# Optimization experiments

Measured on AMD Instinct MI355X. Metric: run time of the kernel, lower is better.

Reference implementation:

```python
import jax, jax.numpy as jnp
import numpy as np

PLANES, RATIO = 512, 4
Q = PLANES // RATIO  # 128
B, H, W = 4, 128, 128


def _dw_stride2(x, k):
    # depthwise 3x3 stride-2 conv, NCHW, kernel [C,1,3,3]
    return jax.lax.conv_general_dilated(
        x, k, window_strides=(2, 2), padding=((1, 1), (1, 1)),
        feature_group_count=x.shape[1],
        dimension_numbers=('NCHW', 'OIHW', 'NCHW'))


def _upsample_bilinear_ac(x, out_h, out_w):
    # bilinear, align_corners=True (matches F.interpolate)
    n, c, h, w = x.shape
    def co(out, ins):
        s = (ins - 1) / (out - 1)
        pos = jnp.arange(out, dtype=jnp.float32) * jnp.float32(s)
        i0 = jnp.floor(pos).astype(jnp.int32)
        i1 = jnp.minimum(i0 + 1, ins - 1)
        return i0, i1, pos - i0.astype(jnp.float32)
    y0, y1, ty = co(out_h, h)
    x0, x1, tx = co(out_w, w)
    rows = x[:, :, y0, :] * (1 - ty)[None, None, :, None] + x[:, :, y1, :] * ty[None, None, :, None]
    return rows[:, :, :, x0] * (1 - tx) + rows[:, :, :, x1] * tx


def setup_inputs() -> dict:
    key = jax.random.key(0)
    ks = jax.random.split(key, 32)
    nrm = lambda k, s, sc=0.05: jax.random.normal(k, s, jnp.float32) * sc
    uni = lambda k, s: jax.random.uniform(k, s, jnp.float32, 0.5, 1.5)
    return {
        'feat': jax.random.normal(ks[0], (B, PLANES, H, W), jnp.float32),
        'w_phi': nrm(ks[1], (2 * Q, PLANES)),
        'bn_phi_s': uni(ks[2], (2 * Q,)), 'bn_phi_b': nrm(ks[3], (2 * Q,)),
        'w_theta': nrm(ks[4], (Q, PLANES)),
        'bn_theta_s': uni(ks[5], (Q,)), 'bn_theta_b': nrm(ks[6], (Q,)),
        'w_adj': nrm(ks[7], (Q, Q)),
        'bn_adj_s': uni(ks[8], (Q,)), 'bn_adj_b': nrm(ks[9], (Q,)),
        'w_wg': nrm(ks[10], (2 * Q, 2 * Q)),
        'bn_wg_s': uni(ks[11], (2 * Q,)), 'bn_wg_b': nrm(ks[12], (2 * Q,)),
        'w_conv3': nrm(ks[13], (PLANES, 2 * Q)),
        'bn3_s': uni(ks[14], (PLANES,)), 'bn3_b': nrm(ks[15], (PLANES,)),
        'w_local1': nrm(ks[16], (PLANES, 1, 3, 3), 0.2),
        'bnl1_s': uni(ks[17], (PLANES,)), 'bnl1_b': nrm(ks[18], (PLANES,)),
        'w_local2': nrm(ks[19], (PLANES, 1, 3, 3), 0.2),
        'bnl2_s': uni(ks[20], (PLANES,)), 'bnl2_b': nrm(ks[21], (PLANES,)),
        'w_local3': nrm(ks[22], (PLANES, 1, 3, 3), 0.2),
        'bnl3_s': uni(ks[23], (PLANES,)), 'bnl3_b': nrm(ks[24], (PLANES,)),
        'gamma': nrm(ks[25], (1,), 0.5),
        'w_final': nrm(ks[26], (PLANES, 2 * PLANES)),
        'bnf_s': uni(ks[27], (PLANES,)), 'bnf_b': nrm(ks[28], (PLANES,)),
    }


def reference(feat, w_phi, bn_phi_s, bn_phi_b, w_theta, bn_theta_s, bn_theta_b,
              w_adj, bn_adj_s, bn_adj_b, w_wg, bn_wg_s, bn_wg_b,
              w_conv3, bn3_s, bn3_b,
              w_local1, bnl1_s, bnl1_b, w_local2, bnl2_s, bnl2_b,
              w_local3, bnl3_s, bnl3_b, gamma, w_final, bnf_s, bnf_b):
    n, c, h, w = feat.shape
    bn2 = lambda x, s, b: x * s[None, :, None, None] + b[None, :, None, None]
    bn1 = lambda x, s, b: x * s[None, :, None] + b[None, :, None]
    conv1x1 = lambda x, wt: jnp.einsum('oc,nchw->nohw', wt, x)

    l = bn2(_dw_stride2(feat, w_local1), bnl1_s, bnl1_b)
    l = bn2(_dw_stride2(l, w_local2), bnl2_s, bnl2_b)
    l = bn2(_dw_stride2(l, w_local3), bnl3_s, bnl3_b)
    nl, cl, hl, wl = l.shape
    v = l.reshape(nl, cl, hl * wl)                      # [n,C,hw]
    energy = jnp.einsum('nck,ndk->ncd', v, v)           # [n,C,C]
    attn = jax.nn.softmax(jnp.max(energy, -1, keepdims=True) - energy, axis=-1)
    cam = jnp.einsum('ncd,ndk->nck', attn, v).reshape(nl, cl, hl, wl)
    l = gamma * cam + l
    local = _upsample_bilinear_ac(l, h, w)
    spatial_local_feat = feat * local + feat

    # ---- graph branch
    q = w_theta.shape[0]
    x_sqz = bn2(conv1x1(feat, w_phi), bn_phi_s, bn_phi_b).reshape(n, 2 * q, h * w)
    b_m = bn2(conv1x1(feat, w_theta), bn_theta_s, bn_theta_b).reshape(n, q, h * w)
    z_idt = jnp.einsum('nck,ndk->ncd', x_sqz, b_m)      # [n,2q,q]
    z = jnp.swapaxes(z_idt, 1, 2)                       # [n,q,2q]
    z = bn1(jnp.einsum('oi,nil->nol', w_adj, z), bn_adj_s, bn_adj_b)
    z = jnp.swapaxes(z, 1, 2) + z_idt                   # [n,2q,q]
    z = bn1(jnp.einsum('oi,nil->nol', w_wg, z), bn_wg_s, bn_wg_b)
    y = jnp.einsum('ncd,ndk->nck', z, b_m).reshape(n, 2 * q, h, w)
    y = bn2(conv1x1(y, w_conv3), bn3_s, bn3_b)
    g_out = jax.nn.relu(feat + y)

    out = bn2(conv1x1(jnp.concatenate([spatial_local_feat, g_out], axis=1), w_final), bnf_s, bnf_b)
    return out
```

## Files before the change

### kernel.cpp

```cpp
#include <hip/hip_runtime.h>
#include <hip/hip_bf16.h>
#include <cstddef>
#include <cstdint>

static constexpr int NB  = 4;
static constexpr int CH  = 512;
static constexpr int HH  = 128;
static constexpr int WWi = 128;
static constexpr int HW  = HH * WWi;
static constexpr int Qd  = 128;
static constexpr int Q2d = 256;

typedef __attribute__((ext_vector_type(8))) short bf8;
typedef __attribute__((ext_vector_type(4))) float f4;

__device__ __forceinline__ short f2bf(float x) {
  __hip_bfloat16 h = __float2bfloat16(x);
  short s; __builtin_memcpy(&s, &h, 2); return s;
}
__device__ __forceinline__ float bfs2f(short u) {
  union { unsigned int i; float f; } x;
  x.i = ((unsigned int)(unsigned short)u) << 16; return x.f;
}

__launch_bounds__(256)
__global__ void dw_conv_bn4(const float* __restrict__ in, float* __restrict__ out,
                            const float* __restrict__ wgt, const float* __restrict__ s,
                            const float* __restrict__ b, int Hi, int Wi, int Ho, int Wo4) {
  int idx = blockIdx.x * 256 + threadIdx.x;
  int q = idx % Wo4; int t = idx / Wo4;
  int ho = t % Ho; t /= Ho;
  int c = t % CH;
  const float* ip = in + (size_t)t * Hi * Wi;
  const float* wp = wgt + c * 9;
  float w[9];
#pragma unroll
  for (int k = 0; k < 9; k++) w[k] = wp[k];
  const int x0 = q * 8;
  float acc0 = 0.f, acc1 = 0.f, acc2 = 0.f, acc3 = 0.f;
#pragma unroll
  for (int kh = 0; kh < 3; kh++) {
    int y = ho * 2 - 1 + kh;
    if ((unsigned)y < (unsigned)Hi) {
      const float* row = ip + (size_t)y * Wi + x0;
      float4 v0 = *(const float4*)row;
      float4 v1 = *(const float4*)(row + 4);
      float left = (x0 > 0) ? row[-1] : 0.f;
      float xs[9] = {left, v0.x, v0.y, v0.z, v0.w, v1.x, v1.y, v1.z, v1.w};
      const float w0 = w[kh * 3 + 0], w1 = w[kh * 3 + 1], w2 = w[kh * 3 + 2];
      acc0 += w0 * xs[0] + w1 * xs[1] + w2 * xs[2];
      acc1 += w0 * xs[2] + w1 * xs[3] + w2 * xs[4];
      acc2 += w0 * xs[4] + w1 * xs[5] + w2 * xs[6];
      acc3 += w0 * xs[6] + w1 * xs[7] + w2 * xs[8];
    }
  }
  const float sc = s[c], bb = b[c];
  float4 o;
  o.x = acc0 * sc + bb; o.y = acc1 * sc + bb;
  o.z = acc2 * sc + bb; o.w = acc3 * sc + bb;
  *(float4*)(out + (size_t)idx * 4) = o;
}

__launch_bounds__(256)
__global__ void lrow_kernel(const float* __restrict__ lcam, float* __restrict__ lrow) {
  int idx = blockIdx.x * 256 + threadIdx.x;
  int wcol = idx & 127; int t = idx >> 7;
  int hy = t & 15; t >>= 4;
  float pos = wcol * (15.f / 127.f);
  int x0 = (int)pos; if (x0 > 15) x0 = 15;
  float tx = pos - x0;
  int x1 = x0 + 1; if (x1 > 15) x1 = 15;
  const float* lc = lcam + ((size_t)t * 16 + hy) * 16;
  lrow[idx] = lc[x0] * (1.f - tx) + lc[x1] * tx;
}

__launch_bounds__(256)
__global__ void cvt_f32_bf16(const float* __restrict__ in, short* __restrict__ out, int n4) {
  int i = blockIdx.x * 256 + threadIdx.x;
  if (i >= n4) return;
  float4 v = ((const float4*)in)[i];
  short tmp[4] = {f2bf(v.x), f2bf(v.y), f2bf(v.z), f2bf(v.w)};
  short4 o; __builtin_memcpy(&o, tmp, 8);
  ((short4*)out)[i] = o;
}

__launch_bounds__(256)
__global__ void slf_build(const float* __restrict__ feat, const float* __restrict__ lrw,
                          short* __restrict__ slfb, int h0) {
  int idx = blockIdx.x * 256 + threadIdx.x;
  int w8 = (idx & 15) * 8; int t = idx >> 4;
  int h = (t & 63) + h0; t >>= 6;
  const float posy = h * (15.f / 127.f);
  int hy0 = (int)posy; if (hy0 > 15) hy0 = 15;
  int hy1 = hy0 + 1; if (hy1 > 15) hy1 = 15;
  const float tyv = posy - hy0;
  const float* fr = feat + (size_t)t * HW + h * WWi + w8;
  const float* l0r = lrw + ((size_t)t * 16 + hy0) * WWi + w8;
  const float* l1r = lrw + ((size_t)t * 16 + hy1) * WWi + w8;
  float4 f0 = *(const float4*)fr, f1 = *(const float4*)(fr + 4);
  float4 a0 = *(const float4*)l0r, a1 = *(const float4*)(l0r + 4);
  float4 b0 = *(const float4*)l1r, b1 = *(const float4*)(l1r + 4);
  float fv[8], av[8], bv[8];
  __builtin_memcpy(&fv[0], &f0, 16); __builtin_memcpy(&fv[4], &f1, 16);
  __builtin_memcpy(&av[0], &a0, 16); __builtin_memcpy(&av[4], &a1, 16);
  __builtin_memcpy(&bv[0], &b0, 16); __builtin_memcpy(&bv[4], &b1, 16);
  union { short s[8]; bf8 v; } u;
#pragma unroll
  for (int e = 0; e < 8; e++) {
    float v = fv[e] * (1.f + av[e] + (bv[e] - av[e]) * tyv);
    u.s[e] = f2bf(v);
  }
  *(bf8*)(slfb + ((size_t)t * 64 + (h - h0)) * WWi + w8) = u.v;
}

__device__ __forceinline__ int sls(int row, int slot) {
  return row * 64 + ((slot ^ (((row >> 1) ^ (row >> 3)) & 7)) << 3);
}
__device__ __forceinline__ void stg64_b16(const short* __restrict__ src, size_t stride,
                                          int kb, short* lds, int t) {
#pragma unroll
  for (int i = 0; i < 4; i++) {
    int chunk = t + i * 256;
    int row = chunk >> 3, slot = chunk & 7;
    bf8 v = *(const bf8*)(src + (size_t)row * stride + kb + slot * 8);
    *(bf8*)(lds + sls(row, slot)) = v;
  }
}
__device__ __forceinline__ void stg64_f32(const float* __restrict__ src, size_t stride,
                                          int kb, short* lds, int t) {
#pragma unroll
  for (int i = 0; i < 4; i++) {
    int chunk = t + i * 256;
    int row = chunk >> 3, slot = chunk & 7;
    const float* sp = src + (size_t)row * stride + kb + slot * 8;
    float4 v0 = *(const float4*)sp, v1 = *(const float4*)(sp + 4);
    union { short s[8]; bf8 v; } u;
    u.s[0] = f2bf(v0.x); u.s[1] = f2bf(v0.y); u.s[2] = f2bf(v0.z); u.s[3] = f2bf(v0.w);
    u.s[4] = f2bf(v1.x); u.s[5] = f2bf(v1.y); u.s[6] = f2bf(v1.z); u.s[7] = f2bf(v1.w);
    *(bf8*)(lds + sls(row, slot)) = u.v;
  }
}
__device__ __forceinline__ void stg64_t32(const float* __restrict__ src, size_t sstride,
                                          int pb, short* lds, int t) {
#pragma unroll
  for (int i2 = 0; i2 < 4; i2++) {
    int chunk = t + i2 * 256;
    int c = (chunk >> 3) & 63;
    int p8 = ((chunk & 7) | ((chunk >> 6) & 8)) * 8;
    const float* fr = src + (size_t)c * sstride + pb + p8;
    float4 f0 = *(const float4*)fr, f1 = *(const float4*)(fr + 4);
    float fv[8];
    __builtin_memcpy(&fv[0], &f0, 16); __builtin_memcpy(&fv[4], &f1, 16);
    int slot = c >> 3, eidx = c & 7;
#pragma unroll
    for (int e = 0; e < 8; e++) {
      lds[sls(p8 + e, slot) + eidx] = f2bf(fv[e]);
    }
  }
}
__device__ __forceinline__ void stg64_t16(const short* __restrict__ src, size_t sstride,
                                          int pb, short* lds, int t) {
#pragma unroll
  for (int i2 = 0; i2 < 4; i2++) {
    int chunk = t + i2 * 256;
    int c = (chunk >> 3) & 63;
    int p8 = ((chunk & 7) | ((chunk >> 6) & 8)) * 8;
    bf8 v = *(const bf8*)(src + (size_t)c * sstride + pb + p8);
    int slot = c >> 3, eidx = c & 7;
#pragma unroll
    for (int e = 0; e < 8; e++) {
      lds[sls(p8 + e, slot) + eidx] = v[e];
    }
  }
}
__device__ __forceinline__ bf8 fragld64(const short* lds, int row, int kk, int lg) {
  return *(const bf8*)(lds + sls(row, kk * 4 + lg));
}

__launch_bounds__(256)
__global__ void energy_mfma(const float* __restrict__ l3, float* __restrict__ energy) {
  const int c0 = blockIdx.x * 128;
  const int d0 = blockIdx.y * 128;
  const int n = blockIdx.z;
  const int t = threadIdx.x;
  const int lane16 = t & 15, lg = (t >> 4) & 3, wave = t >> 6;
  const int wm = (wave >> 1) * 64, wn = (wave & 1) * 64;
  __shared__ __align__(16) short lA[8192], lB[8192];
  const float* srcA = l3 + ((size_t)n * CH + c0) * 256;
  const float* srcB = l3 + ((size_t)n * CH + d0) * 256;
  f4 acc[4][4];
#pragma unroll
  for (int i = 0; i < 4; i++)
#pragma unroll
    for (int j = 0; j < 4; j++) acc[i][j] = (f4)0.f;
  for (int kb = 0; kb < 256; kb += 64) {
    stg64_f32(srcA, 256, kb, lA, t);
    stg64_f32(srcB, 256, kb, lB, t);
    __syncthreads();
#pragma unroll
    for (int kk = 0; kk < 2; kk++) {
      bf8 av[4], bv[4];
#pragma unroll
      for (int i = 0; i < 4; i++) av[i] = fragld64(lA, wm + i * 16 + lane16, kk, lg);
#pragma unroll
      for (int j = 0; j < 4; j++) bv[j] = fragld64(lB, wn + j * 16 + lane16, kk, lg);
#pragma unroll
      for (int i = 0; i < 4; i++)
#pragma unroll
        for (int j = 0; j < 4; j++)
          acc[i][j] = __builtin_amdgcn_mfma_f32_16x16x32_bf16(av[i], bv[j], acc[i][j], 0, 0, 0);
    }
    __syncthreads();
  }
#pragma unroll
  for (int i = 0; i < 4; i++)
#pragma unroll
    for (int j = 0; j < 4; j++) {
      int d = d0 + wn + j * 16 + lane16;
#pragma unroll
      for (int r = 0; r < 4; r++) {
        int c = c0 + wm + i * 16 + lg * 4 + r;
        energy[((size_t)n * CH + c) * CH + d] = acc[i][j][r];
      }
    }
}

__launch_bounds__(256)
__global__ void softmax_attn(float* __restrict__ energy) {
  float* row = energy + (size_t)blockIdx.x * CH;
  int t = threadIdx.x;
  __shared__ float red[256];
  float e0 = row[t], e1 = row[t + 256];
  red[t] = fminf(e0, e1);
  __syncthreads();
  for (int s = 128; s > 0; s >>= 1) {
    if (t < s) red[t] = fminf(red[t], red[t + s]);
    __syncthreads();
  }
  float emin = red[0];
  __syncthreads();
  float w0 = __expf(emin - e0), w1 = __expf(emin - e1);
  red[t] = w0 + w1;
  __syncthreads();
  for (int s = 128; s > 0; s >>= 1) {
    if (t < s) red[t] += red[t + s];
    __syncthreads();
  }
  float inv = 1.f / red[0];
  row[t] = w0 * inv;
  row[t + 256] = w1 * inv;
}

__launch_bounds__(256)
__global__ void cam_mfma(const float* __restrict__ attn, const float* __restrict__ l3,
                         const float* __restrict__ gamma, float* __restrict__ lcam) {
  const int pb = blockIdx.x * 128;
  const int mb = blockIdx.y * 128;
  const int n = blockIdx.z;
  const int t = threadIdx.x;
  const int lane16 = t & 15, lg = (t >> 4) & 3, wave = t >> 6;
  const int wm = (wave >> 1) * 64, wn = (wave & 1) * 64;
  __shared__ __align__(16) short lA[8192], lB[8192];
  const float* srcA = attn + ((size_t)n * CH + mb) * CH;
  const float gm = gamma[0];
  f4 acc[4][4];
#pragma unroll
  for (int i = 0; i < 4; i++)
#pragma unroll
    for (int j = 0; j < 4; j++) acc[i][j] = (f4)0.f;
  for (int kb = 0; kb < 512; kb += 64) {
    stg64_f32(srcA, CH, kb, lA, t);
    stg64_t32(l3 + ((size_t)n * CH + kb) * 256, 256, pb, lB, t);
    __syncthreads();
#pragma unroll
    for (int kk = 0; kk < 2; kk++) {
      bf8 av[4], bv[4];
#pragma unroll
      for (int i = 0; i < 4; i++) av[i] = fragld64(lA, wm + i * 16 + lane16, kk, lg);
#pragma unroll
      for (int j = 0; j < 4; j++) bv[j] = fragld64(lB, wn + j * 16 + lane16, kk, lg);
#pragma unroll
      for (int i = 0; i < 4; i++)
#pragma unroll
        for (int j = 0; j < 4; j++)
          acc[i][j] = __builtin_amdgcn_mfma_f32_16x16x32_bf16(av[i], bv[j], acc[i][j], 0, 0, 0);
    }
    __syncthreads();
  }
#pragma unroll
  for (int i = 0; i < 4; i++)
#pragma unroll
    for (int j = 0; j < 4; j++) {
      int p = pb + wn + j * 16 + lane16;
#pragma unroll
      for (int r = 0; r < 4; r++) {
        int c = mb + wm + i * 16 + lg * 4 + r;
        size_t idx = ((size_t)n * CH + c) * 256 + p;
        lcam[idx] = gm * acc[i][j][r] + l3[idx];
      }
    }
}

__launch_bounds__(256)
__global__ void theta_mfma2(const short* __restrict__ wthb, const float* __restrict__ feat,
                            const float* __restrict__ s, const float* __restrict__ b,
                            short* __restrict__ bmb) {
  const int pb = blockIdx.x * 128;
  const int n = blockIdx.y;
  const int t = threadIdx.x;
  const int lane16 = t & 15, lg = (t >> 4) & 3, wave = t >> 6;
  const int wm = (wave >> 1) * 64, wn = (wave & 1) * 64;
  __shared__ __align__(16) short lA[8192], lB[8192];
  f4 acc[4][4];
#pragma unroll
  for (int i = 0; i < 4; i++)
#pragma unroll
    for (int j = 0; j < 4; j++) acc[i][j] = (f4)0.f;
  for (int kb = 0; kb < 512; kb += 64) {
    stg64_b16(wthb, 512, kb, lA, t);
    stg64_t32(feat + ((size_t)(n * CH) + kb) * HW, HW, pb, lB, t);
    __syncthreads();
#pragma unroll
    for (int kk = 0; kk < 2; kk++) {
      bf8 av[4], bv[4];
#pragma unroll
      for (int i = 0; i < 4; i++) av[i] = fragld64(lA, wm + i * 16 + lane16, kk, lg);
#pragma unroll
      for (int j = 0; j < 4; j++) bv[j] = fragld64(lB, wn + j * 16 + lane16, kk, lg);
#pragma unroll
      for (int i = 0; i < 4; i++)
#pragma unroll
        for (int j = 0; j < 4; j++)
          acc[i][j] = __builtin_amdgcn_mfma_f32_16x16x32_bf16(av[i], bv[j], acc[i][j], 0, 0, 0);
    }
    __syncthreads();
  }
#pragma unroll
  for (int i = 0; i < 4; i++)
#pragma unroll
    for (int j = 0; j < 4; j++) {
      int p = pb + wn + j * 16 + lane16;
#pragma unroll
      for (int r = 0; r < 4; r++) {
        int d = wm + i * 16 + lg * 4 + r;
        bmb[((size_t)(n * Qd) + d) * HW + p] = f2bf(s[d] * acc[i][j][r] + b[d]);
      }
    }
}

__launch_bounds__(256)
__global__ void rowsum_bf(const short* __restrict__ bmb, float* __restrict__ rs) {
  int row = blockIdx.x;
  int t = threadIdx.x;
  const short* r = bmb + (size_t)row * HW;
  float a = 0.f;
  for (int p = t * 8; p < HW; p += 2048) {
    bf8 v = *(const bf8*)(r + p);
#pragma unroll
    for (int e = 0; e < 8; e++) a += bfs2f(v[e]);
  }
  __shared__ float red[256];
  red[t] = a;
  __syncthreads();
  for (int s = 128; s > 0; s >>= 1) {
    if (t < s) red[t] += red[t + s];
    __syncthreads();
  }
  if (t == 0) rs[row] = red[0];
}

__launch_bounds__(256)
__global__ void m1_mfma2(const float* __restrict__ feat, const short* __restrict__ bmb,
                         float* __restrict__ m1p) {
  const int c0 = blockIdx.x * 128;
  const int kc = blockIdx.y;
  const int n = blockIdx.z;
  const int t = threadIdx.x;
  const int lane16 = t & 15, lg = (t >> 4) & 3, wave = t >> 6;
  const int wm = (wave >> 1) * 64, wn = (wave & 1) * 64;
  __shared__ __align__(16) short lA[8192], lB[8192];
  const float* srcA = feat + ((size_t)(n * CH) + c0) * HW;
  const short* srcB = bmb + (size_t)(n * Qd) * HW;
  f4 acc[4][4];
#pragma unroll
  for (int i = 0; i < 4; i++)
#pragma unroll
    for (int j = 0; j < 4; j++) acc[i][j] = (f4)0.f;
  const int kend = kc * 512 + 512;
  for (int kb = kc * 512; kb < kend; kb += 64) {
    stg64_f32(srcA, HW, kb, lA, t);
    stg64_b16(srcB, HW, kb, lB, t);
    __syncthreads();
#pragma unroll
    for (int kk = 0; kk < 2; kk++) {
      bf8 av[4], bv[4];
#pragma unroll
      for (int i = 0; i < 4; i++) av[i] = fragld64(lA, wm + i * 16 + lane16, kk, lg);
#pragma unroll
      for (int j = 0; j < 4; j++) bv[j] = fragld64(lB, wn + j * 16 + lane16, kk, lg);
#pragma unroll
      for (int i = 0; i < 4; i++)
#pragma unroll
        for (int j = 0; j < 4; j++)
          acc[i][j] = __builtin_amdgcn_mfma_f32_16x16x32_bf16(av[i], bv[j], acc[i][j], 0, 0, 0);
    }
    __syncthreads();
  }
#pragma unroll
  for (int i = 0; i < 4; i++)
#pragma unroll
    for (int j = 0; j < 4; j++) {
      int d = wn + j * 16 + lane16;
#pragma unroll
      for (int r = 0; r < 4; r++) {
        int c = c0 + wm + i * 16 + lg * 4 + r;
        m1p[(((size_t)kc * NB + n) * CH + c) * Qd + d] = acc[i][j][r];
      }
    }
}

__launch_bounds__(256)
__global__ void m1_reduce(const float* __restrict__ m1p, float* __restrict__ m1) {
  int idx = blockIdx.x * 256 + threadIdx.x;
  float a = 0.f;
#pragma unroll
  for (int kc = 0; kc < 32; kc++) a += m1p[(size_t)kc * (NB * CH * Qd) + idx];
  m1[idx] = a;
}

__launch_bounds__(128)
__global__ void zidt_kernel(const float* __restrict__ m1, const float* __restrict__ wphi,
                            const float* __restrict__ sp, const float* __restrict__ bp,
                            const float* __restrict__ rs, float* __restrict__ zidt) {
  int n = blockIdx.y, c = blockIdx.x, d = threadIdx.x;
  __shared__ float wrow[512];
  for (int i = d; i < 512; i += 128) wrow[i] = wphi[(size_t)c * 512 + i];
  __syncthreads();
  const float* mb = m1 + (size_t)n * CH * Qd;
  float acc = 0.f;
#pragma unroll 4
  for (int i = 0; i < 512; i++) acc += wrow[i] * mb[i * Qd + d];
  zidt[((size_t)n * Q2d + c) * Qd + d] = sp[c] * acc + bp[c] * rs[n * Qd + d];
}

__launch_bounds__(128)
__global__ void z3_kernel(const float* __restrict__ zidt, const float* __restrict__ wadj,
                          const float* __restrict__ sa, const float* __restrict__ ba,
                          float* __restrict__ z3) {
  int n = blockIdx.y, c = blockIdx.x, d = threadIdx.x;
  __shared__ float zr[128];
  zr[d] = zidt[((size_t)n * Q2d + c) * Qd + d];
  __syncthreads();
  const float* wrow = wadj + (size_t)d * 128;
  float acc = 0.f;
#pragma unroll 4
  for (int i = 0; i < 128; i++) acc += wrow[i] * zr[i];
  z3[((size_t)n * Q2d + c) * Qd + d] = sa[d] * acc + ba[d] + zr[d];
}

__launch_bounds__(128)
__global__ void z4_kernel(const float* __restrict__ z3, const float* __restrict__ wwg,
                          const float* __restrict__ sw, const float* __restrict__ bw,
                          float* __restrict__ z4) {
  int n = blockIdx.y, o = blockIdx.x, d = threadIdx.x;
  __shared__ float wrow[256];
  wrow[d] = wwg[(size_t)o * 256 + d];
  wrow[d + 128] = wwg[(size_t)o * 256 + 128 + d];
  __syncthreads();
  const float* zb = z3 + (size_t)n * Q2d * Qd;
  float acc = 0.f;
#pragma unroll 4
  for (int i = 0; i < 256; i++) acc += wrow[i] * zb[i * Qd + d];
  z4[((size_t)n * Q2d + o) * Qd + d] = sw[o] * acc + bw[o];
}

__launch_bounds__(128)
__global__ void wz_kernel(const float* __restrict__ z4, const float* __restrict__ wc3,
                          const float* __restrict__ s3, float* __restrict__ wz) {
  int n = blockIdx.y, o = blockIdx.x, d = threadIdx.x;
  __shared__ float wrow[256];
  wrow[d] = wc3[(size_t)o * 256 + d];
  wrow[d + 128] = wc3[(size_t)o * 256 + 128 + d];
  __syncthreads();
  const float* zb = z4 + (size_t)n * Q2d * Qd;
  float acc = 0.f;
#pragma unroll 4
  for (int i = 0; i < 256; i++) acc += wrow[i] * zb[i * Qd + d];
  wz[((size_t)n * CH + o) * Qd + d] = s3[o] * acc;
}

__launch_bounds__(256)
__global__ void ygout_mfma2(const float* __restrict__ wz, const short* __restrict__ bmb,
                            const float* __restrict__ feat, const float* __restrict__ b3,
                            short* __restrict__ gout) {
  const int pb = blockIdx.x * 128;
  const int mb = blockIdx.y * 128;
  const int n = blockIdx.z;
  const int t = threadIdx.x;
  const int lane16 = t & 15, lg = (t >> 4) & 3, wave = t >> 6;
  const int wm = (wave >> 1) * 64, wn = (wave & 1) * 64;
  __shared__ __align__(16) short lA[8192], lB[8192];
  const float* srcA = wz + ((size_t)(n * CH) + mb) * Qd;
  f4 acc[4][4];
#pragma unroll
  for (int i = 0; i < 4; i++)
#pragma unroll
    for (int j = 0; j < 4; j++) acc[i][j] = (f4)0.f;
  for (int kb = 0; kb < 128; kb += 64) {
    stg64_f32(srcA, Qd, kb, lA, t);
    stg64_t16(bmb + ((size_t)(n * Qd) + kb) * HW, HW, pb, lB, t);
    __syncthreads();
#pragma unroll
    for (int kk = 0; kk < 2; kk++) {
      bf8 av[4], bv[4];
#pragma unroll
      for (int i = 0; i < 4; i++) av[i] = fragld64(lA, wm + i * 16 + lane16, kk, lg);
#pragma unroll
      for (int j = 0; j < 4; j++) bv[j] = fragld64(lB, wn + j * 16 + lane16, kk, lg);
#pragma unroll
      for (int i = 0; i < 4; i++)
#pragma unroll
        for (int j = 0; j < 4; j++)
          acc[i][j] = __builtin_amdgcn_mfma_f32_16x16x32_bf16(av[i], bv[j], acc[i][j], 0, 0, 0);
    }
    __syncthreads();
  }
#pragma unroll
  for (int i = 0; i < 4; i++)
#pragma unroll
    for (int j = 0; j < 4; j++) {
      int p = pb + wn + j * 16 + lane16;
#pragma unroll
      for (int r = 0; r < 4; r++) {
        int c = mb + wm + i * 16 + lg * 4 + r;
        size_t base = ((size_t)(n * CH) + c) * HW + p;
        float g = feat[base] + acc[i][j][r] + b3[c];
        gout[base] = f2bf(g > 0.f ? g : 0.f);
      }
    }
}

__launch_bounds__(256)
__global__ void final_mfma(const short* __restrict__ wfb, const short* __restrict__ slfb,
                           const int h0, const short* __restrict__ gout,
                           const float* __restrict__ fs, const float* __restrict__ fb,
                           float* __restrict__ out) {
  const int h = blockIdx.x + h0;
  const int pb = h * WWi;
  const int mb = blockIdx.y * 128;
  const int n = blockIdx.z;
  const int t = threadIdx.x;
  const int lane16 = t & 15, lg = (t >> 4) & 3, wave = t >> 6;
  const int wm = (wave >> 1) * 64, wn = (wave & 1) * 64;
  __shared__ __align__(16) short lA[8192], lB[8192];
  f4 acc[4][4];
#pragma unroll
  for (int i = 0; i < 4; i++)
#pragma unroll
    for (int j = 0; j < 4; j++) acc[i][j] = (f4)0.f;

  for (int kb = 0; kb < 1024; kb += 64) {
    stg64_b16(wfb + (size_t)mb * 1024, 1024, kb, lA, t);
    if (kb < 512) {
      stg64_t16(slfb + ((size_t)(n * CH) + kb) * (64 * WWi) + (size_t)(h - h0) * WWi,
                64 * WWi, 0, lB, t);
    } else {
      stg64_t16(gout + ((size_t)(n * CH) + (kb - 512)) * HW, HW, pb, lB, t);
    }
    __syncthreads();
#pragma unroll
    for (int kk = 0; kk < 2; kk++) {
      bf8 avf[4], bvf[4];
#pragma unroll
      for (int i = 0; i < 4; i++) avf[i] = fragld64(lA, wm + i * 16 + lane16, kk, lg);
#pragma unroll
      for (int j = 0; j < 4; j++) bvf[j] = fragld64(lB, wn + j * 16 + lane16, kk, lg);
#pragma unroll
      for (int i = 0; i < 4; i++)
#pragma unroll
        for (int j = 0; j < 4; j++)
          acc[i][j] = __builtin_amdgcn_mfma_f32_16x16x32_bf16(avf[i], bvf[j], acc[i][j], 0, 0, 0);
    }
    __syncthreads();
  }
#pragma unroll
  for (int i = 0; i < 4; i++)
#pragma unroll
    for (int j = 0; j < 4; j++) {
      int p = pb + wn + j * 16 + lane16;
#pragma unroll
      for (int r = 0; r < 4; r++) {
        int m = mb + wm + i * 16 + lg * 4 + r;
        out[((size_t)(n * CH) + m) * HW + p] = fs[m] * acc[i][j][r] + fb[m];
      }
    }
}

extern "C" void kernel_launch(void* const* d_in, const int* in_sizes, int n_in,
                              void* d_out, int out_size, void* d_ws, size_t ws_size,
                              hipStream_t stream) {
  (void)in_sizes; (void)n_in; (void)out_size; (void)ws_size;
  const float* feat      = (const float*)d_in[0];
  const float* w_phi     = (const float*)d_in[1];
  const float* bn_phi_s  = (const float*)d_in[2];
  const float* bn_phi_b  = (const float*)d_in[3];
  const float* w_theta   = (const float*)d_in[4];
  const float* bn_theta_s= (const float*)d_in[5];
  const float* bn_theta_b= (const float*)d_in[6];
  const float* w_adj     = (const float*)d_in[7];
  const float* bn_adj_s  = (const float*)d_in[8];
  const float* bn_adj_b  = (const float*)d_in[9];
  const float* w_wg      = (const float*)d_in[10];
  const float* bn_wg_s   = (const float*)d_in[11];
  const float* bn_wg_b   = (const float*)d_in[12];
  const float* w_conv3   = (const float*)d_in[13];
  const float* bn3_s     = (const float*)d_in[14];
  const float* bn3_b     = (const float*)d_in[15];
  const float* w_l1      = (const float*)d_in[16];
  const float* bnl1_s    = (const float*)d_in[17];
  const float* bnl1_b    = (const float*)d_in[18];
  const float* w_l2      = (const float*)d_in[19];
  const float* bnl2_s    = (const float*)d_in[20];
  const float* bnl2_b    = (const float*)d_in[21];
  const float* w_l3      = (const float*)d_in[22];
  const float* bnl3_s    = (const float*)d_in[23];
  const float* bnl3_b    = (const float*)d_in[24];
  const float* gamma     = (const float*)d_in[25];
  const float* w_final   = (const float*)d_in[26];
  const float* bnf_s     = (const float*)d_in[27];
  const float* bnf_b     = (const float*)d_in[28];

  float* out = (float*)d_out;
  float* l1 = out;
  float* l2 = l1 + (size_t)8388608;
  float* l3 = l2 + (size_t)2097152;
  short* wthb = (short*)(l3 + (size_t)524288);

  float* ws   = (float*)d_ws;
  float* lcam = ws;
  float* lrw  = lcam + (size_t)4 * 512 * 256;
  float* bm_region = lrw + (size_t)4 * 512 * 16 * 128;
  short* bmb  = (short*)bm_region;
  float* rsum = bm_region + (size_t)4 * 128 * 16384;
  float* M1   = rsum + 512;
  float* M1p_old = M1 + (size_t)4 * 512 * 128;
  float* zidt = M1p_old + (size_t)8 * 4 * 512 * 128;
  float* z3b  = zidt + (size_t)4 * 256 * 128;
  float* z4b  = z3b + (size_t)4 * 256 * 128;
  float* wzb  = z4b + (size_t)4 * 256 * 128;
  short* gout = (short*)(wzb + (size_t)4 * 512 * 128);
  short* wfb  = (short*)M1p_old;
  float* m1p  = (float*)gout;
  float* energy = (float*)M1p_old;
  short* slfb = (short*)bm_region;

  dw_conv_bn4<<<dim3(4 * 512 * 64 * 16 / 256), 256, 0, stream>>>(feat, l1, w_l1, bnl1_s, bnl1_b, 128, 128, 64, 16);
  dw_conv_bn4<<<dim3(4 * 512 * 32 * 8 / 256), 256, 0, stream>>>(l1, l2, w_l2, bnl2_s, bnl2_b, 64, 64, 32, 8);
  dw_conv_bn4<<<dim3(4 * 512 * 16 * 4 / 256), 256, 0, stream>>>(l2, l3, w_l3, bnl3_s, bnl3_b, 32, 32, 16, 4);
  energy_mfma<<<dim3(4, 4, 4), 256, 0, stream>>>(l3, energy);
  softmax_attn<<<dim3(4 * 512), 256, 0, stream>>>(energy);
  cam_mfma<<<dim3(2, 4, 4), 256, 0, stream>>>(energy, l3, gamma, lcam);
  lrow_kernel<<<dim3(4 * 512 * 16 * 128 / 256), 256, 0, stream>>>(lcam, lrw);

  cvt_f32_bf16<<<dim3(64), 256, 0, stream>>>(w_theta, wthb, 16384);
  theta_mfma2<<<dim3(128, 4), 256, 0, stream>>>(wthb, feat, bn_theta_s, bn_theta_b, bmb);
  rowsum_bf<<<dim3(512), 256, 0, stream>>>(bmb, rsum);
  m1_mfma2<<<dim3(4, 32, 4), 256, 0, stream>>>(feat, bmb, m1p);
  m1_reduce<<<dim3(1024), 256, 0, stream>>>(m1p, M1);
  zidt_kernel<<<dim3(256, 4), 128, 0, stream>>>(M1, w_phi, bn_phi_s, bn_phi_b, rsum, zidt);
  z3_kernel<<<dim3(256, 4), 128, 0, stream>>>(zidt, w_adj, bn_adj_s, bn_adj_b, z3b);
  z4_kernel<<<dim3(256, 4), 128, 0, stream>>>(z3b, w_wg, bn_wg_s, bn_wg_b, z4b);
  wz_kernel<<<dim3(512, 4), 128, 0, stream>>>(z4b, w_conv3, bn3_s, wzb);
  ygout_mfma2<<<dim3(128, 4, 4), 256, 0, stream>>>(wzb, bmb, feat, bn3_b, gout);

  cvt_f32_bf16<<<dim3(512), 256, 0, stream>>>(w_final, wfb, 131072);

  slf_build<<<dim3(8192), 256, 0, stream>>>(feat, lrw, slfb, 0);
  final_mfma<<<dim3(64, 4, 4), 256, 0, stream>>>(wfb, slfb, 0, gout, bnf_s, bnf_b, out);
  slf_build<<<dim3(8192), 256, 0, stream>>>(feat, lrw, slfb, 64);
  final_mfma<<<dim3(64, 4, 4), 256, 0, stream>>>(wfb, slfb, 64, gout, bnf_s, bnf_b, out);
}
```

Measured before the change: 464.7 us.

## Store slf and gout channel-minor so final GEMM loads B tiles directly

```diff
diff --git a/kernel.cpp b/kernel.cpp
--- a/kernel.cpp
+++ b/kernel.cpp
@@ -84,35 +84,6 @@
   ((short4*)out)[i] = o;
 }
 
-__launch_bounds__(256)
-__global__ void slf_build(const float* __restrict__ feat, const float* __restrict__ lrw,
-                          short* __restrict__ slfb, int h0) {
-  int idx = blockIdx.x * 256 + threadIdx.x;
-  int w8 = (idx & 15) * 8; int t = idx >> 4;
-  int h = (t & 63) + h0; t >>= 6;
-  const float posy = h * (15.f / 127.f);
-  int hy0 = (int)posy; if (hy0 > 15) hy0 = 15;
-  int hy1 = hy0 + 1; if (hy1 > 15) hy1 = 15;
-  const float tyv = posy - hy0;
-  const float* fr = feat + (size_t)t * HW + h * WWi + w8;
-  const float* l0r = lrw + ((size_t)t * 16 + hy0) * WWi + w8;
-  const float* l1r = lrw + ((size_t)t * 16 + hy1) * WWi + w8;
-  float4 f0 = *(const float4*)fr, f1 = *(const float4*)(fr + 4);
-  float4 a0 = *(const float4*)l0r, a1 = *(const float4*)(l0r + 4);
-  float4 b0 = *(const float4*)l1r, b1 = *(const float4*)(l1r + 4);
-  float fv[8], av[8], bv[8];
-  __builtin_memcpy(&fv[0], &f0, 16); __builtin_memcpy(&fv[4], &f1, 16);
-  __builtin_memcpy(&av[0], &a0, 16); __builtin_memcpy(&av[4], &a1, 16);
-  __builtin_memcpy(&bv[0], &b0, 16); __builtin_memcpy(&bv[4], &b1, 16);
-  union { short s[8]; bf8 v; } u;
-#pragma unroll
-  for (int e = 0; e < 8; e++) {
-    float v = fv[e] * (1.f + av[e] + (bv[e] - av[e]) * tyv);
-    u.s[e] = f2bf(v);
-  }
-  *(bf8*)(slfb + ((size_t)t * 64 + (h - h0)) * WWi + w8) = u.v;
-}
-
 __device__ __forceinline__ int sls(int row, int slot) {
   return row * 64 + ((slot ^ (((row >> 1) ^ (row >> 3)) & 7)) << 3);
 }
@@ -175,6 +146,52 @@
 }
 __device__ __forceinline__ bf8 fragld64(const short* lds, int row, int kk, int lg) {
   return *(const bf8*)(lds + sls(row, kk * 4 + lg));
+}
+
+__launch_bounds__(256)
+__global__ void slf_build_T(const float* __restrict__ feat, const float* __restrict__ lrw,
+                            short* __restrict__ slfbT, int h0) {
+  const int cb = blockIdx.x * 64;
+  const int hh = blockIdx.y;
+  const int n  = blockIdx.z;
+  const int h  = hh + h0;
+  const int t  = threadIdx.x;
+  __shared__ __align__(16) short lT[8192];
+  const float posy = h * (15.f / 127.f);
+  int hy0 = (int)posy; if (hy0 > 15) hy0 = 15;
+  int hy1 = hy0 + 1; if (hy1 > 15) hy1 = 15;
+  const float tyv = posy - hy0;
+#pragma unroll
+  for (int i2 = 0; i2 < 4; i2++) {
+    int chunk = t + i2 * 256;
+    int c = (chunk >> 3) & 63;
+    int w8 = ((chunk & 7) | ((chunk >> 6) & 8)) * 8;
+    size_t cidx = (size_t)(n * CH) + cb + c;
+    const float* fr = feat + cidx * HW + h * WWi + w8;
+    const float* l0r = lrw + (cidx * 16 + hy0) * WWi + w8;
+    const float* l1r = lrw + (cidx * 16 + hy1) * WWi + w8;
+    float4 f0 = *(const float4*)fr, f1 = *(const float4*)(fr + 4);
+    float4 a0 = *(const float4*)l0r, a1 = *(const float4*)(l0r + 4);
+    float4 b0 = *(const float4*)l1r, b1 = *(const float4*)(l1r + 4);
+    float fv[8], av[8], bv[8];
+    __builtin_memcpy(&fv[0], &f0, 16); __builtin_memcpy(&fv[4], &f1, 16);
+    __builtin_memcpy(&av[0], &a0, 16); __builtin_memcpy(&av[4], &a1, 16);
+    __builtin_memcpy(&bv[0], &b0, 16); __builtin_memcpy(&bv[4], &b1, 16);
+    int slot = c >> 3, eidx = c & 7;
+#pragma unroll
+    for (int e = 0; e < 8; e++) {
+      float v = fv[e] * (1.f + av[e] + (bv[e] - av[e]) * tyv);
+      lT[sls(w8 + e, slot) + eidx] = f2bf(v);
+    }
+  }
+  __syncthreads();
+#pragma unroll
+  for (int i2 = 0; i2 < 4; i2++) {
+    int chunk = t + i2 * 256;
+    int w = chunk >> 3, slot = chunk & 7;
+    bf8 v = *(const bf8*)(lT + sls(w, slot));
+    *(bf8*)(slfbT + (((size_t)(n * 64) + hh) * WWi + w) * CH + cb + slot * 8) = v;
+  }
 }
 
 __launch_bounds__(256)
@@ -492,7 +509,7 @@
 __launch_bounds__(256)
 __global__ void ygout_mfma2(const float* __restrict__ wz, const short* __restrict__ bmb,
                             const float* __restrict__ feat, const float* __restrict__ b3,
-                            short* __restrict__ gout) {
+                            short* __restrict__ goutT) {
   const int pb = blockIdx.x * 128;
   const int mb = blockIdx.y * 128;
   const int n = blockIdx.z;
@@ -530,19 +547,20 @@
 #pragma unroll
     for (int j = 0; j < 4; j++) {
       int p = pb + wn + j * 16 + lane16;
+      int c0 = mb + wm + i * 16 + lg * 4;
+      union { short s[4]; short4 v; } u;
 #pragma unroll
       for (int r = 0; r < 4; r++) {
-        int c = mb + wm + i * 16 + lg * 4 + r;
-        size_t base = ((size_t)(n * CH) + c) * HW + p;
-        float g = feat[base] + acc[i][j][r] + b3[c];
-        gout[base] = f2bf(g > 0.f ? g : 0.f);
+        float g = feat[((size_t)(n * CH) + c0 + r) * HW + p] + acc[i][j][r] + b3[c0 + r];
+        u.s[r] = f2bf(g > 0.f ? g : 0.f);
       }
-    }
-}
-
-__launch_bounds__(256)
-__global__ void final_mfma(const short* __restrict__ wfb, const short* __restrict__ slfb,
-                           const int h0, const short* __restrict__ gout,
+      *(short4*)(goutT + ((size_t)(n * HW) + p) * CH + c0) = u.v;
+    }
+}
+
+__launch_bounds__(256)
+__global__ void final_mfma(const short* __restrict__ wfb, const short* __restrict__ slfbT,
+                           const int h0, const short* __restrict__ goutT,
                            const float* __restrict__ fs, const float* __restrict__ fb,
                            float* __restrict__ out) {
   const int h = blockIdx.x + h0;
@@ -553,6 +571,8 @@
   const int lane16 = t & 15, lg = (t >> 4) & 3, wave = t >> 6;
   const int wm = (wave >> 1) * 64, wn = (wave & 1) * 64;
   __shared__ __align__(16) short lA[8192], lB[8192];
+  const short* slfRows = slfbT + ((size_t)(n * 64) + (h - h0)) * WWi * CH;
+  const short* goutRows = goutT + ((size_t)(n * HW) + pb) * CH;
   f4 acc[4][4];
 #pragma unroll
   for (int i = 0; i < 4; i++)
@@ -562,10 +582,9 @@
   for (int kb = 0; kb < 1024; kb += 64) {
     stg64_b16(wfb + (size_t)mb * 1024, 1024, kb, lA, t);
     if (kb < 512) {
-      stg64_t16(slfb + ((size_t)(n * CH) + kb) * (64 * WWi) + (size_t)(h - h0) * WWi,
-                64 * WWi, 0, lB, t);
+      stg64_b16(slfRows, CH, kb, lB, t);
     } else {
-      stg64_t16(gout + ((size_t)(n * CH) + (kb - 512)) * HW, HW, pb, lB, t);
+      stg64_b16(goutRows, CH, kb - 512, lB, t);
     }
     __syncthreads();
 #pragma unroll
@@ -675,8 +694,8 @@
 
   cvt_f32_bf16<<<dim3(512), 256, 0, stream>>>(w_final, wfb, 131072);
 
-  slf_build<<<dim3(8192), 256, 0, stream>>>(feat, lrw, slfb, 0);
+  slf_build_T<<<dim3(8, 64, 4), 256, 0, stream>>>(feat, lrw, slfb, 0);
   final_mfma<<<dim3(64, 4, 4), 256, 0, stream>>>(wfb, slfb, 0, gout, bnf_s, bnf_b, out);
-  slf_build<<<dim3(8192), 256, 0, stream>>>(feat, lrw, slfb, 64);
+  slf_build_T<<<dim3(8, 64, 4), 256, 0, stream>>>(feat, lrw, slfb, 64);
   final_mfma<<<dim3(64, 4, 4), 256, 0, stream>>>(wfb, slfb, 64, gout, bnf_s, bnf_b, out);
 }
```

After: 462.8 us. About the same (-0.4%).
